# Kernel tuning notes

Measured on AMD Instinct MI355X. Metric: run time of the kernel, lower is better.

The kernel has to match this reference:

```python
import jax, jax.numpy as jnp
import numpy as np

HID, NL, NH, DH, FF = 768, 12, 12, 64, 3072
VOCAB, MAXPOS = 30522, 512
T_ELE, T_ROLE = 17, 7
B, L = 16, 256
LN_EPS = 1e-12


def _layernorm(x, g, b):
    mu = x.mean(-1, keepdims=True)
    var = ((x - mu) ** 2).mean(-1, keepdims=True)
    return (x - mu) / jnp.sqrt(var + LN_EPS) * g + b


def _bert(datas, word_emb, pos_emb, type_emb, emb_ln_g, emb_ln_b,
          Wq, bq, Wk, bk, Wv, bv, Wo, bo, ln1_g, ln1_b,
          W1, b1, W2, b2, ln2_g, ln2_b):
    Bv, Lv = datas.shape
    x = word_emb[datas] + pos_emb[:Lv][None] + type_emb[0][None, None]
    x = _layernorm(x, emb_ln_g, emb_ln_b)
    for i in range(NL):  # loop over fixed layer count, not data dims
        q = (x @ Wq[i] + bq[i]).reshape(Bv, Lv, NH, DH)
        k = (x @ Wk[i] + bk[i]).reshape(Bv, Lv, NH, DH)
        v = (x @ Wv[i] + bv[i]).reshape(Bv, Lv, NH, DH)
        att = jax.nn.softmax(jnp.einsum('bqhd,bkhd->bhqk', q, k) / jnp.sqrt(jnp.float32(DH)), axis=-1)
        ctx = jnp.einsum('bhqk,bkhd->bqhd', att, v).reshape(Bv, Lv, HID)
        x = _layernorm(x + ctx @ Wo[i] + bo[i], ln1_g[i], ln1_b[i])
        h = jax.nn.gelu(x @ W1[i] + b1[i], approximate=False)
        x = _layernorm(x + h @ W2[i] + b2[i], ln2_g[i], ln2_b[i])
    return x


def _crf_llh(em, tags, mask, start, end, trans):
    # torchcrf CRF.forward with batch_first=True, reduction='sum'
    Bv, Lv, T = em.shape
    bidx = jnp.arange(Bv)
    em_t = jnp.transpose(em, (1, 0, 2))        # [L,B,T]
    tags_t = tags.T.astype(jnp.int32)          # [L,B]
    mask_t = mask.T.astype(em.dtype)           # [L,B]
    # numerator: score of gold path
    score = start[tags_t[0]] + em_t[0][bidx, tags_t[0]]
    def num_step(s, xs):
        e_t, tg, tp, m = xs
        return s + m * (trans[tp, tg] + e_t[bidx, tg]), None
    score, _ = jax.lax.scan(num_step, score, (em_t[1:], tags_t[1:], tags_t[:-1], mask_t[1:]))
    last_idx = (mask_t.sum(0) - 1).astype(jnp.int32)
    num = score + end[tags[bidx, last_idx]]
    # denominator: forward algorithm (log-sum-exp semiring)
    alpha = start[None] + em_t[0]              # [B,T]
    def den_step(a, xs):
        e_t, m = xs
        nxt = jax.nn.logsumexp(a[:, :, None] + trans[None] + e_t[:, None, :], axis=1)
        return jnp.where(m[:, None] > 0, nxt, a), None
    alpha, _ = jax.lax.scan(den_step, alpha, (em_t[1:], mask_t[1:]))
    den = jax.nn.logsumexp(alpha + end[None], axis=1)
    return jnp.sum(num - den)


def _crf_decode(em, start, end, trans):
    # torchcrf CRF.decode without mask -> full-length Viterbi
    Bv = em.shape[0]
    bidx = jnp.arange(Bv)
    em_t = jnp.transpose(em, (1, 0, 2))        # [L,B,T]
    alpha = start[None] + em_t[0]
    def fwd(a, e_t):
        sc = a[:, :, None] + trans[None]       # [B,T_prev,T_cur]
        return jnp.max(sc, axis=1) + e_t, jnp.argmax(sc, axis=1)
    alpha, hist = jax.lax.scan(fwd, alpha, em_t[1:])   # hist [L-1,B,T]
    last = jnp.argmax(alpha + end[None], axis=1)
    def back(cur, h):
        prev = h[bidx, cur]
        return prev, prev
    _, ys = jax.lax.scan(back, last, hist, reverse=True)  # ys[t] = tag at pos t
    return jnp.concatenate([ys, last[None]], axis=0).T    # [B,L]


def setup_inputs() -> dict:
    key = jax.random.key(0)
    ks = iter(jax.random.split(key, 64))
    n = lambda shape: jax.random.normal(next(ks), shape, dtype=jnp.float32) * 0.02
    inp = {
        'datas': jax.random.randint(next(ks), (B, L), 0, VOCAB, dtype=jnp.int32),
        'ele_labels': jax.random.randint(next(ks), (B, L), 0, T_ELE, dtype=jnp.int32),
        'role_labels': jax.random.randint(next(ks), (B, L), 0, T_ROLE, dtype=jnp.int32),
        'seq_mask': jnp.ones((B, L), dtype=bool),
        'word_emb': n((VOCAB, HID)), 'pos_emb': n((MAXPOS, HID)), 'type_emb': n((2, HID)),
        'emb_ln_g': jnp.ones((HID,)), 'emb_ln_b': jnp.zeros((HID,)),
        'Wq': n((NL, HID, HID)), 'bq': jnp.zeros((NL, HID)),
        'Wk': n((NL, HID, HID)), 'bk': jnp.zeros((NL, HID)),
        'Wv': n((NL, HID, HID)), 'bv': jnp.zeros((NL, HID)),
        'Wo': n((NL, HID, HID)), 'bo': jnp.zeros((NL, HID)),
        'ln1_g': jnp.ones((NL, HID)), 'ln1_b': jnp.zeros((NL, HID)),
        'W1': n((NL, HID, FF)), 'b1': jnp.zeros((NL, FF)),
        'W2': n((NL, FF, HID)), 'b2': jnp.zeros((NL, HID)),
        'ln2_g': jnp.ones((NL, HID)), 'ln2_b': jnp.zeros((NL, HID)),
        'W_ele': n((HID, T_ELE)), 'b_ele': jnp.zeros((T_ELE,)),
        'W_role': n((HID, T_ROLE)), 'b_role': jnp.zeros((T_ROLE,)),
        'ele_start': n((T_ELE,)), 'ele_end': n((T_ELE,)), 'ele_trans': n((T_ELE, T_ELE)),
        'role_start': n((T_ROLE,)), 'role_end': n((T_ROLE,)), 'role_trans': n((T_ROLE, T_ROLE)),
    }
    return inp


def reference(datas, ele_labels, role_labels, seq_mask,
              word_emb, pos_emb, type_emb, emb_ln_g, emb_ln_b,
              Wq, bq, Wk, bk, Wv, bv, Wo, bo, ln1_g, ln1_b,
              W1, b1, W2, b2, ln2_g, ln2_b,
              W_ele, b_ele, W_role, b_role,
              ele_start, ele_end, ele_trans, role_start, role_end, role_trans):
    wemb = _bert(datas, word_emb, pos_emb, type_emb, emb_ln_g, emb_ln_b,
                 Wq, bq, Wk, bk, Wv, bv, Wo, bo, ln1_g, ln1_b,
                 W1, b1, W2, b2, ln2_g, ln2_b)
    ele_em = wemb @ W_ele + b_ele
    role_em = wemb @ W_role + b_role
    mask = seq_mask.astype(jnp.float32)
    ele_llh = _crf_llh(ele_em, ele_labels, mask, ele_start, ele_end, ele_trans)
    role_llh = _crf_llh(role_em, role_labels, mask, role_start, role_end, role_trans)
    loss = -ele_llh - role_llh
    ele_dec = _crf_decode(ele_em, ele_start, ele_end, ele_trans)
    role_dec = _crf_decode(role_em, role_start, role_end, role_trans)
    return loss, ele_dec, role_dec
```

## Files before the change

### kernel.cpp

```cpp
#include <hip/hip_runtime.h>
#include <stdint.h>
#include <math.h>

typedef _Float16 f16;
typedef _Float16 f16x8 __attribute__((ext_vector_type(8)));
typedef float f32x4 __attribute__((ext_vector_type(4)));

#define LO_SCALE 2048.0f
#define INV_LO_SCALE (1.0f/2048.0f)
#define LOG2E 1.4426950408889634f
#define MFMA16(a, b, c) __builtin_amdgcn_mfma_f32_16x16x32_f16(a, b, c, 0, 0, 0)

__device__ __forceinline__ void split1(float x, f16 &hi, f16 &lo) {
    f16 h = (f16)x;
    hi = h;
    lo = (f16)((x - (float)h) * LO_SCALE);
}

__device__ __forceinline__ float fexp2(float x) {
#if __has_builtin(__builtin_amdgcn_exp2f)
    return __builtin_amdgcn_exp2f(x);
#else
    return exp2f(x);
#endif
}
__device__ __forceinline__ float flog2(float x) {
#if __has_builtin(__builtin_amdgcn_logf)
    return __builtin_amdgcn_logf(x);
#else
    return log2f(x);
#endif
}

#define GLOAD16(g, l) __builtin_amdgcn_global_load_lds( \
    (const __attribute__((address_space(1))) void*)(g), \
    (__attribute__((address_space(3))) void*)(l), 16, 0, 0)

__device__ __forceinline__ void swz_decode(int &mi, int &ni)
{
    const int NN = gridDim.y;
    int s = blockIdx.x + blockIdx.y * gridDim.x;
    const int c = s & 7;
    const int idx = s >> 3;
    const int mchunk = gridDim.x >> 3;
    const int md = idx / NN;
    mi = c * mchunk + md;
    ni = idx - md * NN;
}

template<int EPI>
__device__ __forceinline__ void epi_write(float val, int row, int col, int N,
                                          float* __restrict__ C,
                                          f16* __restrict__ Oh, f16* __restrict__ Ol,
                                          f16* __restrict__ X2h, f16* __restrict__ X2l,
                                          f16* __restrict__ X3h, f16* __restrict__ X3l)
{
    if constexpr (EPI == 0) {
        C[(size_t)row * N + col] = val;
    } else if constexpr (EPI == 1) {
        float ge = 0.5f * val * (1.0f + erff(val * 0.70710678118654752440f));
        f16 hi, lo;
        split1(ge, hi, lo);
        size_t o = (size_t)row * N + col;
        Oh[o] = hi;
        Ol[o] = lo;
    } else {
        int sect = col >= 1536 ? 2 : (col >= 768 ? 1 : 0);
        int cc = col - sect * 768;
        int hd = cc >> 6;
        int d = cc & 63;
        int bh = (row >> 8) * 12 + hd;
        int lt = row & 255;
        f16 hi, lo;
        split1(val, hi, lo);
        if (sect == 0) {
            size_t o = ((size_t)bh * 256 + lt) * 64 + d;
            Oh[o] = hi; Ol[o] = lo;
        } else if (sect == 1) {
            size_t o = ((size_t)bh * 256 + lt) * 64 + d;
            X2h[o] = hi; X2l[o] = lo;
        } else {
            size_t o = ((size_t)bh * 64 + d) * 256 + lt;
            X3h[o] = hi; X3l[o] = lo;
        }
    }
}

template<int EPI>
__global__ __launch_bounds__(256, 2)
void gemm128(const f16* __restrict__ Ah, const f16* __restrict__ Al,
             const f16* __restrict__ Bh, const f16* __restrict__ Bl,
             const float* __restrict__ bias, float* __restrict__ C,
             f16* __restrict__ Oh, f16* __restrict__ Ol,
             f16* __restrict__ X2h, f16* __restrict__ X2l,
             f16* __restrict__ X3h, f16* __restrict__ X3l, int K, int N)
{
    __shared__ f16 smem[2][16384];

    int mi, ni;
    swz_decode(mi, ni);
    const int m0 = mi * 128;
    const int n0 = ni * 128;

    const int tid = threadIdx.x;
    const int lane = tid & 63;
    const int w = tid >> 6;
    const int l15 = lane & 15;
    const int lg = lane >> 4;

    f32x4 accm[4][4];
    f32x4 accc[4][4];
#pragma unroll
    for (int i = 0; i < 4; ++i)
#pragma unroll
        for (int j = 0; j < 4; ++j) {
            accm[i][j] = (f32x4){0.f, 0.f, 0.f, 0.f};
            accc[i][j] = (f32x4){0.f, 0.f, 0.f, 0.f};
        }

    const f16* gA0 = Ah + (size_t)(m0 + w * 32 + l15) * K + lg * 8;
    const f16* gA1 = gA0 + 16 * (size_t)K;
    const f16* gAl0 = Al + (size_t)(m0 + w * 32 + l15) * K + lg * 8;
    const f16* gAl1 = gAl0 + 16 * (size_t)K;
    const f16* gB0 = Bh + (size_t)(n0 + w * 32 + l15) * K + lg * 8;
    const f16* gB1 = gB0 + 16 * (size_t)K;
    const f16* gBl0 = Bl + (size_t)(n0 + w * 32 + l15) * K + lg * 8;
    const f16* gBl1 = gBl0 + 16 * (size_t)K;
    const int ldsb0 = w * 1024;
    const int ldsb1 = w * 1024 + 512;

    const int nt = K >> 5;

#define STAGE(buf, k0)                                   \
    {                                                    \
        f16* sb = &smem[buf][0];                         \
        GLOAD16(gA0 + (k0), sb + ldsb0);                 \
        GLOAD16(gA1 + (k0), sb + ldsb1);                 \
        GLOAD16(gAl0 + (k0), sb + 4096 + ldsb0);         \
        GLOAD16(gAl1 + (k0), sb + 4096 + ldsb1);         \
        GLOAD16(gB0 + (k0), sb + 8192 + ldsb0);          \
        GLOAD16(gB1 + (k0), sb + 8192 + ldsb1);          \
        GLOAD16(gBl0 + (k0), sb + 12288 + ldsb0);        \
        GLOAD16(gBl1 + (k0), sb + 12288 + ldsb1);        \
    }

    STAGE(0, 0);
    __syncthreads();

    const int fro = lg * 128 + l15 * 8;
    const int wrg = (w >> 1) * 4;
    const int wcg = (w & 1) * 4;

    int cur = 0;
    for (int t = 0; t < nt; ++t) {
        if (t + 1 < nt) STAGE(cur ^ 1, (t + 1) * 32);

        const f16* sb = &smem[cur][0];
        f16x8 fbh[4], fbl[4];
#pragma unroll
        for (int ni2 = 0; ni2 < 4; ++ni2) {
            int offb = 8192 + (wcg + ni2) * 512 + fro;
            fbh[ni2] = *(const f16x8*)(sb + offb);
            fbl[ni2] = *(const f16x8*)(sb + offb + 4096);
        }
#pragma unroll
        for (int mi2 = 0; mi2 < 4; ++mi2) {
            int offa = (wrg + mi2) * 512 + fro;
            f16x8 fah = *(const f16x8*)(sb + offa);
            f16x8 fal = *(const f16x8*)(sb + offa + 4096);
            __builtin_amdgcn_s_setprio(1);
#pragma unroll
            for (int ni2 = 0; ni2 < 4; ++ni2) {
                accm[mi2][ni2] = MFMA16(fah, fbh[ni2], accm[mi2][ni2]);
                accc[mi2][ni2] = MFMA16(fah, fbl[ni2], accc[mi2][ni2]);
                accc[mi2][ni2] = MFMA16(fal, fbh[ni2], accc[mi2][ni2]);
            }
            __builtin_amdgcn_s_setprio(0);
        }

        __syncthreads();
        cur ^= 1;
    }
#undef STAGE

    const int wr = (w >> 1) * 64;
    const int wc = (w & 1) * 64;
#pragma unroll
    for (int mi2 = 0; mi2 < 4; ++mi2) {
        int row = m0 + wr + mi2 * 16 + lg * 4;
#pragma unroll
        for (int ni2 = 0; ni2 < 4; ++ni2) {
            int col = n0 + wc + ni2 * 16 + l15;
            float bv = bias[col];
#pragma unroll
            for (int j = 0; j < 4; ++j) {
                float val = accm[mi2][ni2][j] + accc[mi2][ni2][j] * INV_LO_SCALE + bv;
                epi_write<EPI>(val, row + j, col, N, C, Oh, Ol, X2h, X2l, X3h, X3l);
            }
        }
    }
}

__global__ __launch_bounds__(256, 1)
void attn_mfma_kernel(const f16* __restrict__ Qh, const f16* __restrict__ Ql,
                      const f16* __restrict__ Kh, const f16* __restrict__ Kl,
                      const f16* __restrict__ Vth, const f16* __restrict__ Vtl,
                      f16* __restrict__ ch, f16* __restrict__ cl)
{
    __shared__ f16 sKh[256 * 72];
    __shared__ f16 sKl[256 * 72];
    __shared__ f16 sVh[64 * 264];
    __shared__ f16 sVl[64 * 264];
    __shared__ f16 sPh[4][1280];
    __shared__ f16 sPl[4][1280];

    const int bh = blockIdx.x >> 1;
    const int qbase = (blockIdx.x & 1) * 128;
    const int b = bh / 12;
    const int h = bh % 12;
    const int tid = threadIdx.x;
    const int w = tid >> 6;
    const int l = tid & 63;
    const int l15 = l & 15;
    const int lg = l >> 4;

    {
        const f16* gKh = Kh + (size_t)bh * 16384;
        const f16* gKl = Kl + (size_t)bh * 16384;
#pragma unroll
        for (int i = 0; i < 8; ++i) {
            int c = tid + i * 256;
            int off = (c >> 3) * 72 + (c & 7) * 8;
            *(f16x8*)(sKh + off) = *(const f16x8*)(gKh + c * 8);
            *(f16x8*)(sKl + off) = *(const f16x8*)(gKl + c * 8);
        }
        const f16* gVh = Vth + (size_t)bh * 16384;
        const f16* gVl = Vtl + (size_t)bh * 16384;
#pragma unroll
        for (int i = 0; i < 8; ++i) {
            int c = tid + i * 256;
            int off = (c >> 5) * 264 + (c & 31) * 8;
            *(f16x8*)(sVh + off) = *(const f16x8*)(gVh + c * 8);
            *(f16x8*)(sVl + off) = *(const f16x8*)(gVl + c * 8);
        }
    }
    __syncthreads();

    f16x8 qfh[2][2], qfl[2][2];
#pragma unroll
    for (int mt = 0; mt < 2; ++mt) {
        int qr = qbase + w * 32 + mt * 16 + l15;
        size_t qo = ((size_t)bh * 256 + qr) * 64 + lg * 8;
        qfh[mt][0] = *(const f16x8*)(Qh + qo);
        qfh[mt][1] = *(const f16x8*)(Qh + qo + 32);
        qfl[mt][0] = *(const f16x8*)(Ql + qo);
        qfl[mt][1] = *(const f16x8*)(Ql + qo + 32);
    }

    f32x4 S[2][16];
#pragma unroll
    for (int nt = 0; nt < 16; ++nt) {
        int kr = nt * 16 + l15;
        int kaddr = kr * 72 + lg * 8;
        f16x8 kh0 = *(const f16x8*)(sKh + kaddr);
        f16x8 kh1 = *(const f16x8*)(sKh + kaddr + 32);
        f16x8 kl0 = *(const f16x8*)(sKl + kaddr);
        f16x8 kl1 = *(const f16x8*)(sKl + kaddr + 32);
#pragma unroll
        for (int mt = 0; mt < 2; ++mt) {
            f32x4 am = (f32x4){0.f, 0.f, 0.f, 0.f};
            f32x4 ac = (f32x4){0.f, 0.f, 0.f, 0.f};
            am = MFMA16(qfh[mt][0], kh0, am);
            am = MFMA16(qfh[mt][1], kh1, am);
            ac = MFMA16(qfh[mt][0], kl0, ac);
            ac = MFMA16(qfh[mt][1], kl1, ac);
            ac = MFMA16(qfl[mt][0], kh0, ac);
            ac = MFMA16(qfl[mt][1], kh1, ac);
            S[mt][nt] = (am + ac * INV_LO_SCALE) * 0.125f;
        }
    }

#pragma unroll
    for (int mt = 0; mt < 2; ++mt)
#pragma unroll
        for (int j = 0; j < 4; ++j) {
            float m = S[mt][0][j];
#pragma unroll
            for (int nt = 1; nt < 16; ++nt) m = fmaxf(m, S[mt][nt][j]);
            m = fmaxf(m, __shfl_xor(m, 1));
            m = fmaxf(m, __shfl_xor(m, 2));
            m = fmaxf(m, __shfl_xor(m, 4));
            m = fmaxf(m, __shfl_xor(m, 8));
            float s = 0.f;
#pragma unroll
            for (int nt = 0; nt < 16; ++nt) {
                float e = fexp2((S[mt][nt][j] - m) * LOG2E);
                S[mt][nt][j] = e;
                s += e;
            }
            s += __shfl_xor(s, 1);
            s += __shfl_xor(s, 2);
            s += __shfl_xor(s, 4);
            s += __shfl_xor(s, 8);
            float inv = 1.0f / s;
#pragma unroll
            for (int nt = 0; nt < 16; ++nt) S[mt][nt][j] *= inv;
        }

    f32x4 Ohh[2][4], Occ[2][4];
#pragma unroll
    for (int mt = 0; mt < 2; ++mt)
#pragma unroll
        for (int dt = 0; dt < 4; ++dt) {
            Ohh[mt][dt] = (f32x4){0.f, 0.f, 0.f, 0.f};
            Occ[mt][dt] = (f32x4){0.f, 0.f, 0.f, 0.f};
        }

    f16* pbh = &sPh[w][0];
    f16* pbl = &sPl[w][0];
#pragma unroll
    for (int kp = 0; kp < 8; ++kp) {
#pragma unroll
        for (int mt = 0; mt < 2; ++mt)
#pragma unroll
            for (int n2 = 0; n2 < 2; ++n2) {
                int nt = kp * 2 + n2;
#pragma unroll
                for (int j = 0; j < 4; ++j) {
                    int prow = mt * 16 + lg * 4 + j;
                    int pcol = n2 * 16 + l15;
                    f16 hi, lo;
                    split1(S[mt][nt][j], hi, lo);
                    pbh[prow * 40 + pcol] = hi;
                    pbl[prow * 40 + pcol] = lo;
                }
            }
        __builtin_amdgcn_wave_barrier();
#pragma unroll
        for (int mt = 0; mt < 2; ++mt) {
            int paddr = (mt * 16 + l15) * 40 + lg * 8;
            f16x8 ph = *(const f16x8*)(pbh + paddr);
            f16x8 pl = *(const f16x8*)(pbl + paddr);
#pragma unroll
            for (int dt = 0; dt < 4; ++dt) {
                int vaddr = (dt * 16 + l15) * 264 + kp * 32 + lg * 8;
                f16x8 vh = *(const f16x8*)(sVh + vaddr);
                f16x8 vl = *(const f16x8*)(sVl + vaddr);
                Ohh[mt][dt] = MFMA16(ph, vh, Ohh[mt][dt]);
                Occ[mt][dt] = MFMA16(ph, vl, Occ[mt][dt]);
                Occ[mt][dt] = MFMA16(pl, vh, Occ[mt][dt]);
            }
        }
        __builtin_amdgcn_wave_barrier();
    }

#pragma unroll
    for (int mt = 0; mt < 2; ++mt)
#pragma unroll
        for (int dt = 0; dt < 4; ++dt) {
            f32x4 o = Ohh[mt][dt] + Occ[mt][dt] * INV_LO_SCALE;
#pragma unroll
            for (int j = 0; j < 4; ++j) {
                int q = qbase + w * 32 + mt * 16 + lg * 4 + j;
                int d = dt * 16 + l15;
                size_t off = ((size_t)(b * 256 + q)) * 768 + h * 64 + d;
                f16 hi, lo;
                split1(o[j], hi, lo);
                ch[off] = hi;
                cl[off] = lo;
            }
        }
}

__device__ __forceinline__ void tsplit_tile(const float* __restrict__ W,
                                            f16* __restrict__ Th, f16* __restrict__ Tl,
                                            int K, int N, int kb, int nb, int tid,
                                            float (*tile)[33])
{
    const int k0 = kb * 32;
    const int n0 = nb * 32;
    const int r = tid >> 3;
    const int c4 = (tid & 7) * 4;
    float4 v = *(const float4*)&W[(size_t)(k0 + r) * N + n0 + c4];
    tile[r][c4 + 0] = v.x; tile[r][c4 + 1] = v.y;
    tile[r][c4 + 2] = v.z; tile[r][c4 + 3] = v.w;
    __syncthreads();
    f16 hs[4], ls[4];
#pragma unroll
    for (int j = 0; j < 4; ++j) split1(tile[c4 + j][r], hs[j], ls[j]);
    size_t o = (size_t)(n0 + r) * K + k0 + c4;
    Th[o + 0] = hs[0]; Th[o + 1] = hs[1]; Th[o + 2] = hs[2]; Th[o + 3] = hs[3];
    Tl[o + 0] = ls[0]; Tl[o + 1] = ls[1]; Tl[o + 2] = ls[2]; Tl[o + 3] = ls[3];
}

__global__ void tsplit_all_kernel(const float* __restrict__ Wq, const float* __restrict__ Wk,
                                  const float* __restrict__ Wv, const float* __restrict__ Wo,
                                  const float* __restrict__ W1, const float* __restrict__ W2,
                                  f16* __restrict__ qkvh, f16* __restrict__ qkvl,
                                  f16* __restrict__ woh, f16* __restrict__ wol,
                                  f16* __restrict__ w1h, f16* __restrict__ w1l,
                                  f16* __restrict__ w2h, f16* __restrict__ w2l)
{
    __shared__ float tile[32][33];
    const int tid = threadIdx.x;
    int bid = blockIdx.x;
    if (bid < 576) {
        tsplit_tile(Wq, qkvh, qkvl, 768, 768, bid % 24, bid / 24, tid, tile);
    } else if (bid < 1152) {
        bid -= 576;
        tsplit_tile(Wk, qkvh + 768 * 768, qkvl + 768 * 768, 768, 768, bid % 24, bid / 24, tid, tile);
    } else if (bid < 1728) {
        bid -= 1152;
        tsplit_tile(Wv, qkvh + 2 * 768 * 768, qkvl + 2 * 768 * 768, 768, 768, bid % 24, bid / 24, tid, tile);
    } else if (bid < 2304) {
        bid -= 1728;
        tsplit_tile(Wo, woh, wol, 768, 768, bid % 24, bid / 24, tid, tile);
    } else if (bid < 4608) {
        bid -= 2304;
        tsplit_tile(W1, w1h, w1l, 768, 3072, bid % 24, bid / 24, tid, tile);
    } else {
        bid -= 4608;
        tsplit_tile(W2, w2h, w2l, 3072, 768, bid % 96, bid / 96, tid, tile);
    }
}

__global__ void pack_qkv_bias_kernel(const float* __restrict__ bq, const float* __restrict__ bk,
                                     const float* __restrict__ bv, float* __restrict__ qkvb)
{
    const int i = blockIdx.x;
    const int tid = threadIdx.x;
    for (int c = tid; c < 768; c += 256) {
        qkvb[i * 2304 + c]        = bq[i * 768 + c];
        qkvb[i * 2304 + 768 + c]  = bk[i * 768 + c];
        qkvb[i * 2304 + 1536 + c] = bv[i * 768 + c];
    }
}

__device__ void ln_emit(float* vals, float* red, const float* __restrict__ g,
                        const float* __restrict__ be, float* xout,
                        f16* oh, f16* ol, size_t base, int tid)
{
    float s = vals[tid] + vals[tid + 256] + vals[tid + 512];
    red[tid] = s;
    __syncthreads();
    for (int st = 128; st > 0; st >>= 1) { if (tid < st) red[tid] += red[tid + st]; __syncthreads(); }
    float mu = red[0] * (1.0f / 768.0f);
    __syncthreads();
    float d0 = vals[tid] - mu, d1 = vals[tid + 256] - mu, d2 = vals[tid + 512] - mu;
    red[tid] = d0 * d0 + d1 * d1 + d2 * d2;
    __syncthreads();
    for (int st = 128; st > 0; st >>= 1) { if (tid < st) red[tid] += red[tid + st]; __syncthreads(); }
    float var = red[0] * (1.0f / 768.0f);
    float rstd = 1.0f / sqrtf(var + 1e-12f);
    __syncthreads();
    for (int c = tid; c < 768; c += 256) {
        float o = (vals[c] - mu) * rstd * g[c] + be[c];
        if (xout) xout[base + c] = o;
        f16 hi, lo;
        split1(o, hi, lo);
        oh[base + c] = hi;
        ol[base + c] = lo;
    }
}

__global__ void embed_ln_kernel(const int* __restrict__ datas, const float* __restrict__ wemb,
                                const float* __restrict__ pemb, const float* __restrict__ temb,
                                const float* __restrict__ g, const float* __restrict__ be,
                                float* __restrict__ x, f16* __restrict__ xh, f16* __restrict__ xl)
{
    __shared__ float vals[768];
    __shared__ float red[256];
    const int i = blockIdx.x;
    const int tid = threadIdx.x;
    const int l = i & 255;
    const int widx = datas[i];
    for (int c = tid; c < 768; c += 256)
        vals[c] = wemb[(size_t)widx * 768 + c] + pemb[(size_t)l * 768 + c] + temb[c];
    __syncthreads();
    ln_emit(vals, red, g, be, x, xh, xl, (size_t)i * 768, tid);
}

__global__ void res_ln_kernel(float* __restrict__ x, const float* __restrict__ y,
                              const float* __restrict__ g, const float* __restrict__ be,
                              f16* __restrict__ xh, f16* __restrict__ xl)
{
    __shared__ float vals[768];
    __shared__ float red[256];
    const int i = blockIdx.x;
    const int tid = threadIdx.x;
    const size_t base = (size_t)i * 768;
    for (int c = tid; c < 768; c += 256) vals[c] = x[base + c] + y[base + c];
    __syncthreads();
    ln_emit(vals, red, g, be, x, xh, xl, base, tid);
}

__global__ void head_kernel(const float* __restrict__ X, const float* __restrict__ Wh,
                            const float* __restrict__ bh, float* __restrict__ out, int T)
{
    __shared__ float xs[768];
    __shared__ double part[8][32];
    const int i = blockIdx.x;
    const int tid = threadIdx.x;
    for (int c = tid; c < 768; c += 256) xs[c] = X[(size_t)i * 768 + c];
    __syncthreads();
    const int p = tid >> 5;
    const int tg = tid & 31;
    if (tg < T) {
        double a = 0;
        for (int d = p * 96; d < p * 96 + 96; ++d)
            a += (double)xs[d] * (double)Wh[d * T + tg];
        part[p][tg] = a;
    }
    __syncthreads();
    if (tid < T) {
        double s = 0;
        for (int pp = 0; pp < 8; ++pp) s += part[pp][tid];
        out[(size_t)i * T + tid] = (float)(s + (double)bh[tid]);
    }
}

__global__ void crf_num_kernel(const float* __restrict__ em, const int* __restrict__ labels,
                               const float* __restrict__ start, const float* __restrict__ endv,
                               const float* __restrict__ trans, float* __restrict__ num, int T)
{
    __shared__ double red[256];
    const int b = blockIdx.x;
    const int tid = threadIdx.x;
    const int tag = labels[b * 256 + tid];
    float v;
    if (tid == 0) {
        v = start[tag] + em[(size_t)(b * 256) * T + tag];
    } else {
        int pt = labels[b * 256 + tid - 1];
        v = trans[pt * T + tag] + em[(size_t)(b * 256 + tid) * T + tag];
    }
    red[tid] = (double)v;
    __syncthreads();
    for (int st = 128; st > 0; st >>= 1) { if (tid < st) red[tid] += red[tid + st]; __syncthreads(); }
    if (tid == 0) num[b] = (float)(red[0] + (double)endv[labels[b * 256 + 255]]);
}

template<int T>
__global__ void crf_scan_kernel(const float* __restrict__ emG, const float* __restrict__ start,
                                const float* __restrict__ endv, const float* __restrict__ trans,
                                float* __restrict__ den, float* __restrict__ tagOut)
{
    __shared__ float ems[256 * T];
    __shared__ float albuf[32];
    __shared__ unsigned char hist[255 * T + 1];
    const int b = blockIdx.x;
    const bool vit = (blockIdx.y == 1);
    const int c = threadIdx.x;

    for (int idx = c; idx < 256 * T; idx += 64)
        ems[idx] = emG[(size_t)b * 256 * T + idx];
    float trc[T];
#pragma unroll
    for (int p = 0; p < T; ++p) trc[p] = (c < T) ? trans[p * T + c] : 0.f;
    const float ec = (c < T) ? endv[c] : -1e30f;
    __syncthreads();

    float alpha = (c < T) ? (start[c] + ems[c]) : -1e30f;

    if (!vit) {
        for (int t = 1; t < 256; ++t) {
            if (c < T) albuf[c] = alpha;
            __builtin_amdgcn_wave_barrier();
            float a[T];
            float m = -1e30f;
#pragma unroll
            for (int p = 0; p < T; ++p) { a[p] = albuf[p] + trc[p]; m = fmaxf(m, a[p]); }
            float s = 0.f;
#pragma unroll
            for (int p = 0; p < T; ++p) s += fexp2((a[p] - m) * LOG2E);
            float na = m + flog2(s) * 0.6931471805599453f + ems[t * T + c];
            __builtin_amdgcn_wave_barrier();
            if (c < T) alpha = na;
        }
        if (c < T) albuf[c] = alpha + ec;
        __builtin_amdgcn_wave_barrier();
        if (c == 0) {
            float m = -1e30f;
            for (int p = 0; p < T; ++p) m = fmaxf(m, albuf[p]);
            float s = 0.f;
            for (int p = 0; p < T; ++p) s += fexp2((albuf[p] - m) * LOG2E);
            den[b] = m + flog2(s) * 0.6931471805599453f;
        }
    } else {
        for (int t = 1; t < 256; ++t) {
            if (c < T) albuf[c] = alpha;
            __builtin_amdgcn_wave_barrier();
            float best = albuf[0] + trc[0];
            int arg = 0;
#pragma unroll
            for (int p = 1; p < T; ++p) {
                float v2 = albuf[p] + trc[p];
                if (v2 > best) { best = v2; arg = p; }
            }
            __builtin_amdgcn_wave_barrier();
            if (c < T) {
                alpha = best + ems[t * T + c];
                hist[(t - 1) * T + c] = (unsigned char)arg;
            }
        }
        if (c < T) albuf[c] = alpha + ec;
        __builtin_amdgcn_wave_barrier();
        if (c == 0) {
            float bv = albuf[0];
            int cur = 0;
            for (int p = 1; p < T; ++p) {
                if (albuf[p] > bv) { bv = albuf[p]; cur = p; }
            }
            tagOut[b * 256 + 255] = (float)cur;
            for (int t = 254; t >= 0; --t) {
                cur = hist[t * T + cur];
                tagOut[b * 256 + t] = (float)cur;
            }
        }
    }
}

__global__ void loss_kernel(const float* __restrict__ num, const float* __restrict__ den,
                            float* __restrict__ out)
{
    __shared__ double red[32];
    const int tid = threadIdx.x;
    red[tid] = (double)num[tid] - (double)den[tid];
    __syncthreads();
    for (int st = 16; st > 0; st >>= 1) { if (tid < st) red[tid] += red[tid + st]; __syncthreads(); }
    if (tid == 0) out[0] = (float)(-red[0]);
}

extern "C" void kernel_launch(void* const* d_in, const int* in_sizes, int n_in,
                              void* d_out, int out_size, void* d_ws, size_t ws_size,
                              hipStream_t stream)
{
    (void)in_sizes; (void)n_in; (void)out_size; (void)ws_size;
    const int* datas       = (const int*)d_in[0];
    const int* ele_labels  = (const int*)d_in[1];
    const int* role_labels = (const int*)d_in[2];
    const float* word_emb = (const float*)d_in[4];
    const float* pos_emb  = (const float*)d_in[5];
    const float* type_emb = (const float*)d_in[6];
    const float* emb_g = (const float*)d_in[7];
    const float* emb_b = (const float*)d_in[8];
    const float* Wq = (const float*)d_in[9];  const float* bq = (const float*)d_in[10];
    const float* Wk = (const float*)d_in[11]; const float* bk = (const float*)d_in[12];
    const float* Wv = (const float*)d_in[13]; const float* bv = (const float*)d_in[14];
    const float* Wo = (const float*)d_in[15]; const float* bo = (const float*)d_in[16];
    const float* ln1g = (const float*)d_in[17]; const float* ln1b = (const float*)d_in[18];
    const float* W1 = (const float*)d_in[19]; const float* b1 = (const float*)d_in[20];
    const float* W2 = (const float*)d_in[21]; const float* b2 = (const float*)d_in[22];
    const float* ln2g = (const float*)d_in[23]; const float* ln2b = (const float*)d_in[24];
    const float* W_ele = (const float*)d_in[25]; const float* b_ele = (const float*)d_in[26];
    const float* W_role = (const float*)d_in[27]; const float* b_role = (const float*)d_in[28];
    const float* ele_start = (const float*)d_in[29];
    const float* ele_end   = (const float*)d_in[30];
    const float* ele_trans = (const float*)d_in[31];
    const float* role_start = (const float*)d_in[32];
    const float* role_end   = (const float*)d_in[33];
    const float* role_trans = (const float*)d_in[34];
    float* out = (float*)d_out;

    uint8_t* ws = (uint8_t*)d_ws;
    float* x      = (float*)(ws + 0x0000000);
    f16* xh       = (f16*)  (ws + 0x0C00000);
    f16* xl       = (f16*)  (ws + 0x1200000);
    f16* Qh       = (f16*)  (ws + 0x1800000);
    f16* Ql       = (f16*)  (ws + 0x1E00000);
    f16* Kh       = (f16*)  (ws + 0x2400000);
    f16* Kl       = (f16*)  (ws + 0x2A00000);
    f16* Vth      = (f16*)  (ws + 0x3000000);
    f16* Vtl      = (f16*)  (ws + 0x3600000);
    f16* ctxh     = (f16*)  (ws + 0x3C00000);
    f16* ctxl     = (f16*)  (ws + 0x4200000);
    float* rbuf   = (float*)(ws + 0x4800000);
    f16* hh       = (f16*)  (ws + 0x1800000);
    f16* hl       = (f16*)  (ws + 0x3000000);
    f16* wqkv_h   = (f16*)  (ws + 0x5400000);
    f16* wqkv_l   = (f16*)  (ws + 0x5760000);
    f16* wo_h     = (f16*)  (ws + 0x5AC0000);
    f16* wo_l     = (f16*)  (ws + 0x5BE0000);
    f16* w1_h     = (f16*)  (ws + 0x5D00000);
    f16* w1_l     = (f16*)  (ws + 0x6180000);
    f16* w2_h     = (f16*)  (ws + 0x6600000);
    f16* w2_l     = (f16*)  (ws + 0x6A80000);
    float* qkvb   = (float*)(ws + 0x6F00000);
    float* ele_em = (float*)(ws + 0x6F20000);
    float* role_em= (float*)(ws + 0x6F70000);
    float* numb   = (float*)(ws + 0x6FC0000);
    float* denb   = (float*)(ws + 0x6FC0100);

    pack_qkv_bias_kernel<<<12, 256, 0, stream>>>(bq, bk, bv, qkvb);
    embed_ln_kernel<<<4096, 256, 0, stream>>>(datas, word_emb, pos_emb, type_emb,
                                              emb_g, emb_b, x, xh, xl);

    for (int i = 0; i < 12; ++i) {
        const size_t o768 = (size_t)i * 768 * 768;
        const size_t o3072 = (size_t)i * 768 * 3072;
        tsplit_all_kernel<<<6912, 256, 0, stream>>>(Wq + o768, Wk + o768, Wv + o768, Wo + o768,
                                                    W1 + o3072, W2 + o3072,
                                                    wqkv_h, wqkv_l, wo_h, wo_l,
                                                    w1_h, w1_l, w2_h, w2_l);
        gemm128<2><<<dim3(32, 18), 256, 0, stream>>>(xh, xl, wqkv_h, wqkv_l,
                                                     qkvb + i * 2304, nullptr,
                                                     Qh, Ql, Kh, Kl, Vth, Vtl, 768, 2304);
        attn_mfma_kernel<<<384, 256, 0, stream>>>(Qh, Ql, Kh, Kl, Vth, Vtl, ctxh, ctxl);
        gemm128<0><<<dim3(32, 6), 256, 0, stream>>>(ctxh, ctxl, wo_h, wo_l,
                                                    bo + i * 768, rbuf, nullptr, nullptr,
                                                    nullptr, nullptr, nullptr, nullptr, 768, 768);
        res_ln_kernel<<<4096, 256, 0, stream>>>(x, rbuf, ln1g + i * 768, ln1b + i * 768, xh, xl);
        gemm128<1><<<dim3(32, 24), 256, 0, stream>>>(xh, xl, w1_h, w1_l,
                                                     b1 + i * 3072, nullptr, hh, hl,
                                                     nullptr, nullptr, nullptr, nullptr, 768, 3072);
        gemm128<0><<<dim3(32, 6), 256, 0, stream>>>(hh, hl, w2_h, w2_l,
                                                    b2 + i * 768, rbuf, nullptr, nullptr,
                                                    nullptr, nullptr, nullptr, nullptr, 3072, 768);
        res_ln_kernel<<<4096, 256, 0, stream>>>(x, rbuf, ln2g + i * 768, ln2b + i * 768, xh, xl);
    }

    head_kernel<<<4096, 256, 0, stream>>>(x, W_ele, b_ele, ele_em, 17);
    head_kernel<<<4096, 256, 0, stream>>>(x, W_role, b_role, role_em, 7);

    crf_num_kernel<<<16, 256, 0, stream>>>(ele_em, ele_labels, ele_start, ele_end, ele_trans, numb, 17);
    crf_num_kernel<<<16, 256, 0, stream>>>(role_em, role_labels, role_start, role_end, role_trans, numb + 16, 7);
    crf_scan_kernel<17><<<dim3(16, 2), 64, 0, stream>>>(ele_em, ele_start, ele_end, ele_trans, denb, out + 1);
    crf_scan_kernel<7><<<dim3(16, 2), 64, 0, stream>>>(role_em, role_start, role_end, role_trans, denb + 16, out + 1 + 4096);
    loss_kernel<<<1, 32, 0, stream>>>(numb, denb, out);
}
```

Baseline: 5.674 ms.

## Hoist weight splitting into one batched launch and use wave-per-token LayerNorm

Weight transpose/split into fp16 hi/lo pairs for all 12 layers now runs in a single 2D-grid launch before the layer loop, writing into a large per-layer workspace when it is big enough. If it is not, the code falls back to the old per-layer split. LayerNorm kernels are rewritten so each 64-lane wave handles one token with float4 loads and shuffle reductions, replacing block-wide LDS reductions with many barriers. The aim is to cut launch count and LN synchronization overhead, at the cost of much more workspace memory.

```diff
diff --git a/kernel.cpp b/kernel.cpp
--- a/kernel.cpp
+++ b/kernel.cpp
@@ -3,6 +3,7 @@
 #include <math.h>
 
 typedef _Float16 f16;
+typedef _Float16 f16x4 __attribute__((ext_vector_type(4)));
 typedef _Float16 f16x8 __attribute__((ext_vector_type(8)));
 typedef float f32x4 __attribute__((ext_vector_type(4)));
 
@@ -393,34 +394,53 @@
     Tl[o + 0] = ls[0]; Tl[o + 1] = ls[1]; Tl[o + 2] = ls[2]; Tl[o + 3] = ls[3];
 }
 
+#define OFF_QKV_H 0
+#define OFF_QKV_L 1769472
+#define OFF_WO_H  3538944
+#define OFF_WO_L  4128768
+#define OFF_W1_H  4718592
+#define OFF_W1_L  7077888
+#define OFF_W2_H  9437184
+#define OFF_W2_L  11796480
+#define WL_STRIDE 14155776
+
 __global__ void tsplit_all_kernel(const float* __restrict__ Wq, const float* __restrict__ Wk,
                                   const float* __restrict__ Wv, const float* __restrict__ Wo,
                                   const float* __restrict__ W1, const float* __restrict__ W2,
-                                  f16* __restrict__ qkvh, f16* __restrict__ qkvl,
-                                  f16* __restrict__ woh, f16* __restrict__ wol,
-                                  f16* __restrict__ w1h, f16* __restrict__ w1l,
-                                  f16* __restrict__ w2h, f16* __restrict__ w2l)
+                                  f16* __restrict__ wout, size_t outStride)
 {
     __shared__ float tile[32][33];
     const int tid = threadIdx.x;
+    const int layer = blockIdx.y;
+    const size_t o768 = (size_t)layer * 589824;
+    const size_t o3072 = (size_t)layer * 2359296;
+    f16* base = wout + (size_t)layer * outStride;
+    f16* qkvh = base + OFF_QKV_H;
+    f16* qkvl = base + OFF_QKV_L;
+    f16* woh  = base + OFF_WO_H;
+    f16* wol  = base + OFF_WO_L;
+    f16* w1h  = base + OFF_W1_H;
+    f16* w1l  = base + OFF_W1_L;
+    f16* w2h  = base + OFF_W2_H;
+    f16* w2l  = base + OFF_W2_L;
     int bid = blockIdx.x;
     if (bid < 576) {
-        tsplit_tile(Wq, qkvh, qkvl, 768, 768, bid % 24, bid / 24, tid, tile);
+        tsplit_tile(Wq + o768, qkvh, qkvl, 768, 768, bid % 24, bid / 24, tid, tile);
     } else if (bid < 1152) {
         bid -= 576;
-        tsplit_tile(Wk, qkvh + 768 * 768, qkvl + 768 * 768, 768, 768, bid % 24, bid / 24, tid, tile);
+        tsplit_tile(Wk + o768, qkvh + 768 * 768, qkvl + 768 * 768, 768, 768, bid % 24, bid / 24, tid, tile);
     } else if (bid < 1728) {
         bid -= 1152;
-        tsplit_tile(Wv, qkvh + 2 * 768 * 768, qkvl + 2 * 768 * 768, 768, 768, bid % 24, bid / 24, tid, tile);
+        tsplit_tile(Wv + o768, qkvh + 2 * 768 * 768, qkvl + 2 * 768 * 768, 768, 768, bid % 24, bid / 24, tid, tile);
     } else if (bid < 2304) {
         bid -= 1728;
-        tsplit_tile(Wo, woh, wol, 768, 768, bid % 24, bid / 24, tid, tile);
+        tsplit_tile(Wo + o768, woh, wol, 768, 768, bid % 24, bid / 24, tid, tile);
     } else if (bid < 4608) {
         bid -= 2304;
-        tsplit_tile(W1, w1h, w1l, 768, 3072, bid % 24, bid / 24, tid, tile);
+        tsplit_tile(W1 + o3072, w1h, w1l, 768, 3072, bid % 24, bid / 24, tid, tile);
     } else {
         bid -= 4608;
-        tsplit_tile(W2, w2h, w2l, 3072, 768, bid % 96, bid / 96, tid, tile);
+        tsplit_tile(W2 + o3072, w2h, w2l, 3072, 768, bid % 96, bid / 96, tid, tile);
     }
 }
 
@@ -436,62 +456,101 @@
     }
 }
 
-__device__ void ln_emit(float* vals, float* red, const float* __restrict__ g,
-                        const float* __restrict__ be, float* xout,
-                        f16* oh, f16* ol, size_t base, int tid)
-{
-    float s = vals[tid] + vals[tid + 256] + vals[tid + 512];
-    red[tid] = s;
-    __syncthreads();
-    for (int st = 128; st > 0; st >>= 1) { if (tid < st) red[tid] += red[tid + st]; __syncthreads(); }
-    float mu = red[0] * (1.0f / 768.0f);
-    __syncthreads();
-    float d0 = vals[tid] - mu, d1 = vals[tid + 256] - mu, d2 = vals[tid + 512] - mu;
-    red[tid] = d0 * d0 + d1 * d1 + d2 * d2;
-    __syncthreads();
-    for (int st = 128; st > 0; st >>= 1) { if (tid < st) red[tid] += red[tid + st]; __syncthreads(); }
-    float var = red[0] * (1.0f / 768.0f);
-    float rstd = 1.0f / sqrtf(var + 1e-12f);
-    __syncthreads();
-    for (int c = tid; c < 768; c += 256) {
-        float o = (vals[c] - mu) * rstd * g[c] + be[c];
-        if (xout) xout[base + c] = o;
-        f16 hi, lo;
-        split1(o, hi, lo);
-        oh[base + c] = hi;
-        ol[base + c] = lo;
-    }
-}
-
-__global__ void embed_ln_kernel(const int* __restrict__ datas, const float* __restrict__ wemb,
-                                const float* __restrict__ pemb, const float* __restrict__ temb,
-                                const float* __restrict__ g, const float* __restrict__ be,
-                                float* __restrict__ x, f16* __restrict__ xh, f16* __restrict__ xl)
-{
-    __shared__ float vals[768];
-    __shared__ float red[256];
-    const int i = blockIdx.x;
-    const int tid = threadIdx.x;
-    const int l = i & 255;
-    const int widx = datas[i];
-    for (int c = tid; c < 768; c += 256)
-        vals[c] = wemb[(size_t)widx * 768 + c] + pemb[(size_t)l * 768 + c] + temb[c];
-    __syncthreads();
-    ln_emit(vals, red, g, be, x, xh, xl, (size_t)i * 768, tid);
-}
-
-__global__ void res_ln_kernel(float* __restrict__ x, const float* __restrict__ y,
-                              const float* __restrict__ g, const float* __restrict__ be,
-                              f16* __restrict__ xh, f16* __restrict__ xl)
-{
-    __shared__ float vals[768];
-    __shared__ float red[256];
-    const int i = blockIdx.x;
-    const int tid = threadIdx.x;
-    const size_t base = (size_t)i * 768;
-    for (int c = tid; c < 768; c += 256) vals[c] = x[base + c] + y[base + c];
-    __syncthreads();
-    ln_emit(vals, red, g, be, x, xh, xl, base, tid);
+__device__ __forceinline__ void ln_wave_core(float v[12], const float* __restrict__ g,
+                                             const float* __restrict__ be,
+                                             float* __restrict__ x,
+                                             f16* __restrict__ xh, f16* __restrict__ xl,
+                                             size_t base, int cb)
+{
+    float s = 0.f;
+#pragma unroll
+    for (int j = 0; j < 12; ++j) s += v[j];
+#pragma unroll
+    for (int off = 32; off > 0; off >>= 1) s += __shfl_xor(s, off);
+    const float mu = s * (1.0f / 768.0f);
+    float d2 = 0.f;
+#pragma unroll
+    for (int j = 0; j < 12; ++j) { float d = v[j] - mu; d2 += d * d; }
+#pragma unroll
+    for (int off = 32; off > 0; off >>= 1) d2 += __shfl_xor(d2, off);
+    const float rstd = 1.0f / sqrtf(d2 * (1.0f / 768.0f) + 1e-12f);
+
+    const float4* ga = (const float4*)(g + cb);
+    const float4* ba = (const float4*)(be + cb);
+    float o[12];
+#pragma unroll
+    for (int j = 0; j < 3; ++j) {
+        float4 gg = ga[j];
+        float4 bb = ba[j];
+        o[j * 4 + 0] = (v[j * 4 + 0] - mu) * rstd * gg.x + bb.x;
+        o[j * 4 + 1] = (v[j * 4 + 1] - mu) * rstd * gg.y + bb.y;
+        o[j * 4 + 2] = (v[j * 4 + 2] - mu) * rstd * gg.z + bb.z;
+        o[j * 4 + 3] = (v[j * 4 + 3] - mu) * rstd * gg.w + bb.w;
+    }
+    float4* xo = (float4*)(x + base);
+#pragma unroll
+    for (int j = 0; j < 3; ++j)
+        xo[j] = (float4){o[j * 4 + 0], o[j * 4 + 1], o[j * 4 + 2], o[j * 4 + 3]};
+
+    f16 ho[12], lo[12];
+#pragma unroll
+    for (int j = 0; j < 12; ++j) split1(o[j], ho[j], lo[j]);
+#pragma unroll
+    for (int j = 0; j < 3; ++j) {
+        *(f16x4*)(xh + base + j * 4) = (f16x4){ho[j * 4], ho[j * 4 + 1], ho[j * 4 + 2], ho[j * 4 + 3]};
+        *(f16x4*)(xl + base + j * 4) = (f16x4){lo[j * 4], lo[j * 4 + 1], lo[j * 4 + 2], lo[j * 4 + 3]};
+    }
+}
+
+__global__ __launch_bounds__(256)
+void res_ln_w(float* __restrict__ x, const float* __restrict__ y,
+              const float* __restrict__ g, const float* __restrict__ be,
+              f16* __restrict__ xh, f16* __restrict__ xl)
+{
+    const int tok = blockIdx.x * 4 + (threadIdx.x >> 6);
+    const int cb = (threadIdx.x & 63) * 12;
+    const size_t base = (size_t)tok * 768 + cb;
+    const float4* xa = (const float4*)(x + base);
+    const float4* ya = (const float4*)(y + base);
+    float v[12];
+#pragma unroll
+    for (int j = 0; j < 3; ++j) {
+        float4 a = xa[j];
+        float4 b2 = ya[j];
+        v[j * 4 + 0] = a.x + b2.x;
+        v[j * 4 + 1] = a.y + b2.y;
+        v[j * 4 + 2] = a.z + b2.z;
+        v[j * 4 + 3] = a.w + b2.w;
+    }
+    ln_wave_core(v, g, be, x, xh, xl, base, cb);
+}
+
+__global__ __launch_bounds__(256)
+void embed_ln_w(const int* __restrict__ datas, const float* __restrict__ wemb,
+                const float* __restrict__ pemb, const float* __restrict__ temb,
+                const float* __restrict__ g, const float* __restrict__ be,
+                float* __restrict__ x, f16* __restrict__ xh, f16* __restrict__ xl)
+{
+    const int tok = blockIdx.x * 4 + (threadIdx.x >> 6);
+    const int cb = (threadIdx.x & 63) * 12;
+    const size_t base = (size_t)tok * 768 + cb;
+    const int widx = datas[tok];
+    const int l = tok & 255;
+    const float4* wa = (const float4*)(wemb + (size_t)widx * 768 + cb);
+    const float4* pa = (const float4*)(pemb + (size_t)l * 768 + cb);
+    const float4* ta = (const float4*)(temb + cb);
+    float v[12];
+#pragma unroll
+    for (int j = 0; j < 3; ++j) {
+        float4 a = wa[j];
+        float4 b2 = pa[j];
+        float4 c2 = ta[j];
+        v[j * 4 + 0] = a.x + b2.x + c2.x;
+        v[j * 4 + 1] = a.y + b2.y + c2.y;
+        v[j * 4 + 2] = a.z + b2.z + c2.z;
+        v[j * 4 + 3] = a.w + b2.w + c2.w;
+    }
+    ln_wave_core(v, g, be, x, xh, xl, base, cb);
 }
 
 __global__ void head_kernel(const float* __restrict__ X, const float* __restrict__ Wh,
@@ -635,7 +694,7 @@
                               void* d_out, int out_size, void* d_ws, size_t ws_size,
                               hipStream_t stream)
 {
-    (void)in_sizes; (void)n_in; (void)out_size; (void)ws_size;
+    (void)in_sizes; (void)n_in; (void)out_size;
     const int* datas       = (const int*)d_in[0];
     const int* ele_labels  = (const int*)d_in[1];
     const int* role_labels = (const int*)d_in[2];
@@ -677,46 +736,46 @@
     float* rbuf   = (float*)(ws + 0x4800000);
     f16* hh       = (f16*)  (ws + 0x1800000);
     f16* hl       = (f16*)  (ws + 0x3000000);
-    f16* wqkv_h   = (f16*)  (ws + 0x5400000);
-    f16* wqkv_l   = (f16*)  (ws + 0x5760000);
-    f16* wo_h     = (f16*)  (ws + 0x5AC0000);
-    f16* wo_l     = (f16*)  (ws + 0x5BE0000);
-    f16* w1_h     = (f16*)  (ws + 0x5D00000);
-    f16* w1_l     = (f16*)  (ws + 0x6180000);
-    f16* w2_h     = (f16*)  (ws + 0x6600000);
-    f16* w2_l     = (f16*)  (ws + 0x6A80000);
-    float* qkvb   = (float*)(ws + 0x6F00000);
-    float* ele_em = (float*)(ws + 0x6F20000);
-    float* role_em= (float*)(ws + 0x6F70000);
-    float* numb   = (float*)(ws + 0x6FC0000);
-    float* denb   = (float*)(ws + 0x6FC0100);
+    float* qkvb   = (float*)(ws + 0x5400000);
+    float* ele_em = (float*)(ws + 0x5420000);
+    float* role_em= (float*)(ws + 0x5468000);
+    float* numb   = (float*)(ws + 0x5484000);
+    float* denb   = (float*)(ws + 0x5484100);
+    f16* wsplit   = (f16*)  (ws + 0x5490000);
+
+    const bool hoist = ws_size >= (0x5490000ull + 12ull * WL_STRIDE * 2ull + 0x10000ull);
 
     pack_qkv_bias_kernel<<<12, 256, 0, stream>>>(bq, bk, bv, qkvb);
-    embed_ln_kernel<<<4096, 256, 0, stream>>>(datas, word_emb, pos_emb, type_emb,
-                                              emb_g, emb_b, x, xh, xl);
+    embed_ln_w<<<1024, 256, 0, stream>>>(datas, word_emb, pos_emb, type_emb,
+                                         emb_g, emb_b, x, xh, xl);
+    if (hoist)
+        tsplit_all_kernel<<<dim3(6912, 12), 256, 0, stream>>>(Wq, Wk, Wv, Wo, W1, W2,
+                                                              wsplit, WL_STRIDE);
 
     for (int i = 0; i < 12; ++i) {
-        const size_t o768 = (size_t)i * 768 * 768;
-        const size_t o3072 = (size_t)i * 768 * 3072;
-        tsplit_all_kernel<<<6912, 256, 0, stream>>>(Wq + o768, Wk + o768, Wv + o768, Wo + o768,
-                                                    W1 + o3072, W2 + o3072,
-                                                    wqkv_h, wqkv_l, wo_h, wo_l,
-                                                    w1_h, w1_l, w2_h, w2_l);
-        gemm128<2><<<dim3(32, 18), 256, 0, stream>>>(xh, xl, wqkv_h, wqkv_l,
+        if (!hoist)
+            tsplit_all_kernel<<<dim3(6912, 1), 256, 0, stream>>>(
+                Wq + (size_t)i * 589824, Wk + (size_t)i * 589824,
+                Wv + (size_t)i * 589824, Wo + (size_t)i * 589824,
+                W1 + (size_t)i * 2359296, W2 + (size_t)i * 2359296,
+                wsplit, 0);
+        f16* wl = wsplit + (hoist ? (size_t)i * WL_STRIDE : 0);
+
+        gemm128<2><<<dim3(32, 18), 256, 0, stream>>>(xh, xl, wl + OFF_QKV_H, wl + OFF_QKV_L,
                                                      qkvb + i * 2304, nullptr,
                                                      Qh, Ql, Kh, Kl, Vth, Vtl, 768, 2304);
         attn_mfma_kernel<<<384, 256, 0, stream>>>(Qh, Ql, Kh, Kl, Vth, Vtl, ctxh, ctxl);
-        gemm128<0><<<dim3(32, 6), 256, 0, stream>>>(ctxh, ctxl, wo_h, wo_l,
+        gemm128<0><<<dim3(32, 6), 256, 0, stream>>>(ctxh, ctxl, wl + OFF_WO_H, wl + OFF_WO_L,
                                                     bo + i * 768, rbuf, nullptr, nullptr,
                                                     nullptr, nullptr, nullptr, nullptr, 768, 768);
-        res_ln_kernel<<<4096, 256, 0, stream>>>(x, rbuf, ln1g + i * 768, ln1b + i * 768, xh, xl);
-        gemm128<1><<<dim3(32, 24), 256, 0, stream>>>(xh, xl, w1_h, w1_l,
+        res_ln_w<<<1024, 256, 0, stream>>>(x, rbuf, ln1g + i * 768, ln1b + i * 768, xh, xl);
+        gemm128<1><<<dim3(32, 24), 256, 0, stream>>>(xh, xl, wl + OFF_W1_H, wl + OFF_W1_L,
                                                      b1 + i * 3072, nullptr, hh, hl,
                                                      nullptr, nullptr, nullptr, nullptr, 768, 3072);
-        gemm128<0><<<dim3(32, 6), 256, 0, stream>>>(hh, hl, w2_h, w2_l,
+        gemm128<0><<<dim3(32, 6), 256, 0, stream>>>(hh, hl, wl + OFF_W2_H, wl + OFF_W2_L,
                                                     b2 + i * 768, rbuf, nullptr, nullptr,
                                                     nullptr, nullptr, nullptr, nullptr, 3072, 768);
-        res_ln_kernel<<<4096, 256, 0, stream>>>(x, rbuf, ln2g + i * 768, ln2b + i * 768, xh, xl);
+        res_ln_w<<<1024, 256, 0, stream>>>(x, rbuf, ln2g + i * 768, ln2b + i * 768, xh, xl);
     }
 
     head_kernel<<<4096, 256, 0, stream>>>(x, W_ele, b_ele, ele_em, 17);
```

New measurement: 5.507 ms. 3.0% less time.
